# Performance work log

Measured on AMD Instinct MI355X. Metric: run time of the kernel, lower is better.

## Reference

```python
import jax, jax.numpy as jnp
import numpy as np

SEQ, BS, DIM = 2048, 2, 256
G, NQ = 2, 8           # n_keys groups, n_queries total
SUB = NQ // G          # queries per group
EPS = 1e-5


def _ln(x, gamma, beta):
    m = jnp.mean(x, axis=-1, keepdims=True)
    v = jnp.mean(jnp.square(x - m), axis=-1, keepdims=True)
    return (x - m) * jax.lax.rsqrt(v + EPS) * gamma + beta


def setup_inputs() -> dict:
    key = jax.random.key(0)
    ks = jax.random.split(key, 16)
    s = 0.02
    return {
        "x":   jax.random.normal(ks[0], (SEQ, BS, DIM), jnp.float32),
        # block layernorms
        "g0": jnp.ones((DIM,), jnp.float32), "b0": jnp.zeros((DIM,), jnp.float32),
        "g1": jnp.ones((DIM,), jnp.float32), "b1": jnp.zeros((DIM,), jnp.float32),
        # attention q/k layernorm (norm_kvs=True)
        "gn": jnp.ones((DIM,), jnp.float32), "bn": jnp.zeros((DIM,), jnp.float32),
        # attention projections (torch Linear: weight [out,in])
        "wk": jax.random.normal(ks[1], (DIM * G, DIM), jnp.float32) * s,
        "bk": jnp.zeros((DIM * G,), jnp.float32),
        "wv": jax.random.normal(ks[2], (DIM * G, DIM), jnp.float32) * s,
        "bv": jnp.zeros((DIM * G,), jnp.float32),
        "wq": jax.random.normal(ks[3], (DIM * NQ, DIM), jnp.float32) * s,
        "bq": jnp.zeros((DIM * NQ,), jnp.float32),
        "wo": jax.random.normal(ks[4], (DIM, DIM * NQ), jnp.float32) * s,
        "bo": jnp.zeros((DIM,), jnp.float32),
        # FFN: BayesLora(dim,2dim) -> relu -> BayesLora(2dim,dim), eval == plain linear
        "w1": jax.random.normal(ks[5], (2 * DIM, DIM), jnp.float32) * s,
        "bf1": jnp.zeros((2 * DIM,), jnp.float32),
        "w2": jax.random.normal(ks[6], (DIM, 2 * DIM), jnp.float32) * s,
        "bf2": jnp.zeros((DIM,), jnp.float32),
    }


def reference(x, g0, b0, g1, b1, gn, bn, wk, bk, wv, bv, wq, bq, wo, bo, w1, bf1, w2, bf2):
    seq, bs, dim = x.shape
    # --- attention (pre-norm) ---
    h = _ln(x, g0, b0)                                        # s b d
    K = (h @ wk.T + bk).reshape(seq, bs, G, dim)              # s b g i
    V = (h @ wv.T + bv).reshape(seq, bs, G, dim)              # s b g i
    Q = (h @ wq.T + bq).reshape(seq, bs, G, SUB, dim)         # s b g u i
    K = _ln(K, gn, bn)
    Q = _ln(Q, gn, bn)
    scores = jnp.einsum('sbgui,tbgi->bgust', Q, K) / jnp.sqrt(jnp.float32(dim))
    neg = jnp.finfo(scores.dtype).min
    causal = jnp.tril(jnp.ones((seq, seq), bool))             # s1 >= s2 allowed
    scores = jnp.where(causal, scores, neg)
    probs = jax.nn.softmax(scores, axis=-1)                   # b g u s t
    out = jnp.einsum('bgust,tbgi->sbgui', probs, V)
    out = out.reshape(seq, bs, G * SUB * dim)                 # s b (g u i)
    x = x + (out @ wo.T + bo)
    # --- FFN (pre-norm) ---
    h2 = _ln(x, g1, b1)
    f = jax.nn.relu(h2 @ w1.T + bf1) @ w2.T + bf2
    return x + f
```

## Files before the change

kernel.cpp:

```cpp
#include <hip/hip_runtime.h>
#include <hip/hip_bf16.h>

#define SEQ  2048
#define BSZ  2
#define DIM  256
#define NG   2
#define NQH  8
#define SUBQ 4
#define ROWS (SEQ*BSZ)
#define NQKV 3072
#define QROW 6144

typedef unsigned int uint32;
typedef unsigned short ushort;
typedef __attribute__((ext_vector_type(8))) short short8;
typedef __attribute__((ext_vector_type(4))) float f32x4;

__device__ __forceinline__ float bflo(uint32 u){
  union { uint32 i; float f; } c; c.i = u << 16; return c.f;
}
__device__ __forceinline__ float bfhi(uint32 u){
  union { uint32 i; float f; } c; c.i = u & 0xffff0000u; return c.f;
}
__device__ __forceinline__ uint32 pack2(float a, float b){
  __hip_bfloat16 ha = __float2bfloat16(a);
  __hip_bfloat16 hb = __float2bfloat16(b);
  unsigned short ua, ub;
  __builtin_memcpy(&ua, &ha, 2);
  __builtin_memcpy(&ub, &hb, 2);
  return (uint32)ua | ((uint32)ub << 16);
}
__device__ __forceinline__ ushort bf16bits(float v){
  __hip_bfloat16 h = __float2bfloat16(v);
  ushort u; __builtin_memcpy(&u, &h, 2); return u;
}

__device__ __forceinline__ void dma16(const void* g, void* l) {
  __builtin_amdgcn_global_load_lds(
      (const __attribute__((address_space(1))) uint32*)g,
      (__attribute__((address_space(3))) uint32*)l, 16, 0, 0);
}

__global__ __launch_bounds__(256) void misc0(
    const float* __restrict__ wk, const float* __restrict__ wv,
    const float* __restrict__ wq, const float* __restrict__ wo,
    const float* __restrict__ w1, const float* __restrict__ w2,
    const float* __restrict__ bk, const float* __restrict__ bv,
    const float* __restrict__ bq,
    __hip_bfloat16* __restrict__ out, float* __restrict__ bc,
    const float* __restrict__ x, const float* __restrict__ g0,
    const float* __restrict__ b0, __hip_bfloat16* __restrict__ Hf)
{
  if (blockIdx.x < 771) {
    int u = blockIdx.x * 256 + threadIdx.x;
    if (u < 196608) {
      int lane = u & 63, col = lane & 15, quad = lane >> 4;
      const float* srcrow;
      if (u < 98304) {
        int n16 = u >> 9, kc = (u >> 6) & 7;
        int n = n16 * 16 + col;
        const float* m = (n < 512) ? (wk + (size_t)n * 256)
                       : (n < 1024) ? (wv + (size_t)(n - 512) * 256)
                                    : (wq + (size_t)(n - 1024) * 256);
        srcrow = m + kc * 32 + quad * 8;
      } else if (u < 163840) {
        int local = u - 98304;
        int n16 = local >> 12, kc = (local >> 6) & 63;
        srcrow = wo + (size_t)(n16 * 16 + col) * 2048 + kc * 32 + quad * 8;
      } else if (u < 180224) {
        int local = u - 163840;
        int n16 = local >> 9, kc = (local >> 6) & 7;
        srcrow = w1 + (size_t)(n16 * 16 + col) * 256 + kc * 32 + quad * 8;
      } else {
        int local = u - 180224;
        int n16 = local >> 10, kc = (local >> 6) & 15;
        srcrow = w2 + (size_t)(n16 * 16 + col) * 512 + kc * 32 + quad * 8;
      }
      float4 a = *(const float4*)srcrow;
      float4 b = *(const float4*)(srcrow + 4);
      uint4 st;
      st.x = pack2(a.x, a.y); st.y = pack2(a.z, a.w);
      st.z = pack2(b.x, b.y); st.w = pack2(b.z, b.w);
      *(uint4*)((ushort*)out + (size_t)u * 8) = st;
    } else {
      int bu = u - 196608;
      const float* src; int loc;
      if      (bu < 128) { src = bk; loc = bu; }
      else if (bu < 256) { src = bv; loc = bu - 128; }
      else               { src = bq; loc = bu - 256; }
      *(float4*)(bc + 4 * (size_t)bu) = *(const float4*)(src + 4 * (size_t)loc);
    }
  } else {
    int wave = threadIdx.x >> 6, lane = threadIdx.x & 63;
    int row = (blockIdx.x - 771) * 4 + wave;
    size_t base = (size_t)row * DIM + lane * 4;
    float4 v = *(const float4*)(x + base);
    float s  = v.x + v.y + v.z + v.w;
    float s2 = v.x*v.x + v.y*v.y + v.z*v.z + v.w*v.w;
    #pragma unroll
    for (int o = 1; o < 64; o <<= 1) {
      s  += __shfl_xor(s, o);
      s2 += __shfl_xor(s2, o);
    }
    float m = s * (1.0f / DIM);
    float rb = rsqrtf(s2 * (1.0f / DIM) - m * m + 1e-5f);
    float4 gm = *(const float4*)(g0 + lane * 4);
    float4 bt = *(const float4*)(b0 + lane * 4);
    uint2 st;
    st.x = pack2((v.x - m) * rb * gm.x + bt.x, (v.y - m) * rb * gm.y + bt.y);
    st.y = pack2((v.z - m) * rb * gm.z + bt.z, (v.w - m) * rb * gm.w + bt.w);
    int kc = lane >> 3, quad = (lane >> 1) & 3, jj = 4 * (lane & 1);
    int cid = (row >> 4) * 8 + kc;
    *(uint2*)((ushort*)Hf + (size_t)cid * 512 + (quad * 16 + (row & 15)) * 8 + jj) = st;
  }
}

__global__ __launch_bounds__(256) void ln_swz(
    __hip_bfloat16* __restrict__ QKV,
    const float* __restrict__ gamma, const float* __restrict__ beta,
    __hip_bfloat16* __restrict__ Kf, __hip_bfloat16* __restrict__ Vf)
{
  int j = blockIdx.x;
  if (j < 10240) {
    int wave = threadIdx.x >> 6, lane = threadIdx.x & 63;
    int idx = j * 4 + wave;
    size_t base;
    if (idx < 8192) base = (size_t)(idx >> 1) * NQKV + (idx & 1) * DIM;
    else {
      int qi = idx - 8192;
      base = (size_t)(qi >> 3) * NQKV + 2 * NG * DIM + (qi & 7) * DIM;
    }
    __hip_bfloat16* p = QKV + base + lane * 4;
    uint2 u = *(const uint2*)p;
    float v0 = bflo(u.x), v1 = bfhi(u.x), v2 = bflo(u.y), v3 = bfhi(u.y);
    float s  = v0 + v1 + v2 + v3;
    float s2 = v0*v0 + v1*v1 + v2*v2 + v3*v3;
    #pragma unroll
    for (int o = 1; o < 64; o <<= 1) {
      s  += __shfl_xor(s, o);
      s2 += __shfl_xor(s2, o);
    }
    float m = s * (1.0f / DIM);
    float rb = rsqrtf(s2 * (1.0f / DIM) - m * m + 1e-5f);
    float4 gm = *(const float4*)(gamma + lane * 4);
    float4 bt = *(const float4*)(beta + lane * 4);
    uint2 st;
    st.x = pack2((v0 - m) * rb * gm.x + bt.x, (v1 - m) * rb * gm.y + bt.y);
    st.y = pack2((v2 - m) * rb * gm.z + bt.z, (v3 - m) * rb * gm.w + bt.w);
    if (idx < 8192) {
      int r = idx >> 1, gg = idx & 1;
      int t = r >> 1, b = r & 1;
      int bg = b * NG + gg;
      int kt = t >> 5, tr = t & 31, tc = tr >> 4, col = tr & 15;
      int ks = lane >> 3, quad = (lane >> 1) & 3, jj = 4 * (lane & 1);
      int cid = (bg * 64 + kt) * 16 + tc * 8 + ks;
      *(uint2*)((ushort*)Kf + (size_t)cid * 512 + (quad * 16 + col) * 8 + jj) = st;
    } else {
      *(uint2*)p = st;
    }
  } else {
    __shared__ ushort T[64][72];
    int vb = j - 10240;
    int t0 = (vb & 31) * 64, d0 = ((vb >> 5) & 3) * 64, bg = vb >> 7;
    int b = bg >> 1, g = bg & 1;
    int tid = threadIdx.x;
    int tr = tid >> 2, c4 = (tid & 3) * 16;
    const ushort* src = (const ushort*)QKV + ((size_t)(t0 + tr) * BSZ + b) * NQKV
                      + NG * DIM + g * DIM + d0 + c4;
    uint4 a0 = *(const uint4*)src;
    uint4 a1 = *(const uint4*)(src + 8);
    *(uint4*)&T[tr][c4]     = a0;
    *(uint4*)&T[tr][c4 + 8] = a1;
    __syncthreads();
    #pragma unroll
    for (int k2 = 0; k2 < 2; ++k2) {
      int u = tid * 2 + k2;
      int tt = u >> 8, di = (u >> 6) & 3, qd = (u >> 4) & 3, cl = u & 15;
      ushort tmp[8];
      #pragma unroll
      for (int e = 0; e < 8; ++e) tmp[e] = T[tt * 32 + qd * 8 + e][di * 16 + cl];
      int kt = (t0 >> 5) + tt;
      int dc = (d0 >> 4) + di;
      *(uint4*)((ushort*)Vf + (((size_t)(bg * 64 + kt) * 16 + dc) << 9) + (qd * 16 + cl) * 8)
          = *(uint4*)tmp;
    }
  }
}

template<int GN, int RELU, int OUTMODE, int AFRAG>
__global__ __launch_bounds__(256) void gemm_mfma(
    const __hip_bfloat16* __restrict__ A,
    const __hip_bfloat16* __restrict__ W,
    const float* __restrict__ bias,
    const float* __restrict__ resid,
    void* __restrict__ outp,
    int M, int N, int K)
{
  constexpr int WCH = GN / 16;
  constexpr int MC  = (GN == 128) ? 4 : 2;
  __shared__ __align__(16) ushort AS[2][4096];
  __shared__ __align__(16) ushort WS[2][WCH * 512];

  const int tid = threadIdx.x;
  const int wave = tid >> 6, lane = tid & 63;
  const int col = lane & 15, quad = lane >> 4;
  const int wm = (GN == 128) ? (wave >> 1) : wave;
  const int wn = (GN == 128) ? (wave & 1) : 0;
  const int bn0 = blockIdx.x * GN;
  const int bm0 = blockIdx.y * 128;
  const bool SPLIT = (OUTMODE == 2 || OUTMODE == 4);
  const int Keff  = SPLIT ? (K / gridDim.z) : K;
  const int kbase = SPLIT ? blockIdx.z * Keff : 0;
  const int kiters = Keff >> 5;

  f32x4 acc[MC][4];
  #pragma unroll
  for (int mc = 0; mc < MC; ++mc)
    #pragma unroll
    for (int nc = 0; nc < 4; ++nc)
      acc[mc][nc] = (f32x4){0.f, 0.f, 0.f, 0.f};

  auto stage = [&](int it, int bufi) {
    int k0 = kbase + it * 32;
    #pragma unroll
    for (int c = 0; c < 2; ++c) {
      int ch = wave * 2 + c;
      if (AFRAG)
        dma16((const ushort*)A + ((((size_t)(bm0 >> 4) + ch) * (K >> 5) + (k0 >> 5)) << 9) + lane * 8,
              &AS[bufi][ch * 512]);
      else
        dma16((const ushort*)A + (size_t)(bm0 + ch * 16 + col) * K + k0 + quad * 8,
              &AS[bufi][ch * 512]);
    }
    #pragma unroll
    for (int c = 0; c < WCH / 4; ++c) {
      int ch = wave * (WCH / 4) + c;
      dma16((const ushort*)W + (((size_t)((bn0 >> 4) + ch) * (K >> 5) + (k0 >> 5)) << 9) + lane * 8,
            &WS[bufi][ch * 512]);
    }
  };

  stage(0, 0);
  for (int it = 0; it < kiters; ++it) {
    int cur = it & 1;
    __syncthreads();
    if (it + 1 < kiters) stage(it + 1, 1 - cur);
    short8 af[MC], bf_[4];
    #pragma unroll
    for (int mc = 0; mc < MC; ++mc)
      af[mc] = *(const short8*)&AS[cur][(wm * MC + mc) * 512 + lane * 8];
    #pragma unroll
    for (int nc = 0; nc < 4; ++nc)
      bf_[nc] = *(const short8*)&WS[cur][(wn * 4 + nc) * 512 + lane * 8];
    #pragma unroll
    for (int mc = 0; mc < MC; ++mc)
      #pragma unroll
      for (int nc = 0; nc < 4; ++nc)
        acc[mc][nc] = __builtin_amdgcn_mfma_f32_16x16x32_bf16(af[mc], bf_[nc], acc[mc][nc], 0, 0, 0);
  }

  #pragma unroll
  for (int nc = 0; nc < 4; ++nc) {
    int n = bn0 + wn * 64 + nc * 16 + col;
    float bv = 0.f;
    if (OUTMODE == 0 || OUTMODE == 1 || OUTMODE == 3) bv = bias[n];
    #pragma unroll
    for (int mc = 0; mc < MC; ++mc) {
      #pragma unroll
      for (int reg = 0; reg < 4; ++reg) {
        int m = bm0 + wm * (MC * 16) + mc * 16 + quad * 4 + reg;
        float v = acc[mc][nc][reg] + bv;
        if ((OUTMODE == 0 || OUTMODE == 1 || OUTMODE == 3) && resid)
          v += resid[(size_t)m * N + n];
        if (RELU) v = fmaxf(v, 0.f);
        if (OUTMODE == 0)
          ((__hip_bfloat16*)outp)[(size_t)m * N + n] = __float2bfloat16(v);
        else if (OUTMODE == 1)
          ((float*)outp)[(size_t)m * N + n] = v;
        else if (OUTMODE == 2)
          ((float*)outp)[(size_t)blockIdx.z * M * N + (size_t)m * N + n] = v;
        else if (OUTMODE == 3) {
          int cid = (m >> 4) * (N >> 5) + (n >> 5);
          int kl = n & 31;
          ((ushort*)outp)[(size_t)cid * 512 + ((kl >> 3) * 16 + (m & 15)) * 8 + (kl & 7)] = bf16bits(v);
        } else {
          ((ushort*)outp)[(size_t)blockIdx.z * M * N + (size_t)m * N + n] = bf16bits(v);
        }
      }
    }
  }
}

__global__ __launch_bounds__(256) void combine2(
    const ushort* __restrict__ P, const float* __restrict__ bias,
    const float* __restrict__ resid, float* __restrict__ out, int MN)
{
  int i4 = (blockIdx.x * 256 + threadIdx.x) * 4;
  uint2 a = *(const uint2*)(P + i4);
  uint2 b = *(const uint2*)(P + MN + i4);
  float4 r = *(const float4*)(resid + i4);
  float4 bb = *(const float4*)(bias + (i4 & (DIM - 1)));
  float4 o;
  o.x = bflo(a.x) + bflo(b.x) + r.x + bb.x;
  o.y = bfhi(a.x) + bfhi(b.x) + r.y + bb.y;
  o.z = bflo(a.y) + bflo(b.y) + r.z + bb.z;
  o.w = bfhi(a.y) + bfhi(b.y) + r.w + bb.w;
  *(float4*)(out + i4) = o;
}

__global__ __launch_bounds__(256) void combine_ln4(
    const ushort* __restrict__ P, const float* __restrict__ bias,
    const float* __restrict__ resid, float* __restrict__ X2,
    const float* __restrict__ gamma, const float* __restrict__ beta,
    __hip_bfloat16* __restrict__ H2f)
{
  const int MN = ROWS * DIM;
  int wave = threadIdx.x >> 6, lane = threadIdx.x & 63;
  int row = blockIdx.x * 4 + wave;
  size_t i = (size_t)row * DIM + lane * 4;
  uint2 a = *(const uint2*)(P + i);
  uint2 b = *(const uint2*)(P + MN + i);
  uint2 c = *(const uint2*)(P + 2 * (size_t)MN + i);
  uint2 d = *(const uint2*)(P + 3 * (size_t)MN + i);
  float4 r = *(const float4*)(resid + i);
  float4 bb = *(const float4*)(bias + lane * 4);
  float4 v;
  v.x = bflo(a.x) + bflo(b.x) + bflo(c.x) + bflo(d.x) + r.x + bb.x;
  v.y = bfhi(a.x) + bfhi(b.x) + bfhi(c.x) + bfhi(d.x) + r.y + bb.y;
  v.z = bflo(a.y) + bflo(b.y) + bflo(c.y) + bflo(d.y) + r.z + bb.z;
  v.w = bfhi(a.y) + bfhi(b.y) + bfhi(c.y) + bfhi(d.y) + r.w + bb.w;
  *(float4*)(X2 + i) = v;
  float s  = v.x + v.y + v.z + v.w;
  float s2 = v.x*v.x + v.y*v.y + v.z*v.z + v.w*v.w;
  #pragma unroll
  for (int o = 1; o < 64; o <<= 1) {
    s  += __shfl_xor(s, o);
    s2 += __shfl_xor(s2, o);
  }
  float m = s * (1.0f / DIM);
  float rb = rsqrtf(s2 * (1.0f / DIM) - m * m + 1e-5f);
  float4 gm = *(const float4*)(gamma + lane * 4);
  float4 bt = *(const float4*)(beta + lane * 4);
  uint2 st;
  st.x = pack2((v.x - m) * rb * gm.x + bt.x, (v.y - m) * rb * gm.y + bt.y);
  st.y = pack2((v.z - m) * rb * gm.z + bt.z, (v.w - m) * rb * gm.w + bt.w);
  int kc = lane >> 3, quad = (lane >> 1) & 3, jj = 4 * (lane & 1);
  int cid = (row >> 4) * 8 + kc;
  *(uint2*)((ushort*)H2f + (size_t)cid * 512 + (quad * 16 + (row & 15)) * 8 + jj) = st;
}

__global__ __launch_bounds__(256, 2) void attn_mfma(
    const __hip_bfloat16* __restrict__ QKV,
    const __hip_bfloat16* __restrict__ Kf,
    const __hip_bfloat16* __restrict__ Vf,
    __hip_bfloat16* __restrict__ Obf,
    __hip_bfloat16* __restrict__ Op1f,
    float* __restrict__ Lp)
{
  __shared__ __align__(16) ushort KS[2][8192];
  __shared__ __align__(16) ushort VS[2][8192];
  __shared__ __align__(16) ushort Pw[4][1280];

  const int tid  = threadIdx.x;
  const int wave = tid >> 6, lane = tid & 63;
  const int col  = lane & 15, quad = lane >> 4;
  const int head = blockIdx.x & 15;
  const int w    = blockIdx.x >> 4;
  int qb, z, split, nit, k0;
  if (w < 24) { qb = 15 - (w >> 1); z = w & 1; split = 1; nit = 2 * qb + 2; k0 = z * nit; }
  else        { qb = 27 - w;        z = 0;     split = 0; nit = 4 * qb + 4; k0 = 0; }

  const int b = head >> 3, hq = head & 7, g = hq >> 2;
  const int bg = b * NG + g;
  const int qw0 = qb * 128 + wave * 32;

  short8 qf[2][8];
  #pragma unroll
  for (int mc = 0; mc < 2; ++mc) {
    int s = qw0 + mc * 16 + col;
    const ushort* qp = (const ushort*)QKV + (size_t)s * QROW + b * NQKV
                     + 2 * NG * DIM + hq * DIM + quad * 8;
    #pragma unroll
    for (int ks = 0; ks < 8; ++ks)
      qf[mc][ks] = *(const short8*)(qp + ks * 32);
  }

  short8 onesf;
  #pragma unroll
  for (int i = 0; i < 8; ++i) onesf[i] = (short)0x3F80;

  f32x4 o[2][16];
  #pragma unroll
  for (int mc = 0; mc < 2; ++mc)
    #pragma unroll
    for (int dc = 0; dc < 16; ++dc)
      o[mc][dc] = (f32x4){0.f, 0.f, 0.f, 0.f};
  float l_s[2][4] = {{0.f}};

  auto stage = [&](int i, int bufi) {
    int kt = k0 + i;
    const ushort* kb = (const ushort*)Kf + (((size_t)bg * 64 + kt) << 13);
    const ushort* vb = (const ushort*)Vf + (((size_t)bg * 64 + kt) << 13);
    #pragma unroll
    for (int cc = 0; cc < 4; ++cc) {
      int nk = wave * 4 + cc;
      dma16(kb + (nk << 9) + lane * 8, &KS[bufi][nk * 512]);
      dma16(vb + (nk << 9) + lane * 8, &VS[bufi][nk * 512]);
    }
  };

  stage(0, 0);
  for (int i = 0; i < nit; ++i) {
    int cur = i & 1;
    __syncthreads();
    if (i + 1 < nit) stage(i + 1, 1 - cur);
    int kt = k0 + i;
    if (kt * 32 > qw0 + 31) continue;

    f32x4 sf[2][2];
    #pragma unroll
    for (int mc = 0; mc < 2; ++mc)
      #pragma unroll
      for (int tc = 0; tc < 2; ++tc)
        sf[mc][tc] = (f32x4){0.f, 0.f, 0.f, 0.f};
    #pragma unroll
    for (int ks = 0; ks < 8; ++ks) {
      short8 kb0 = *(const short8*)&KS[cur][ks * 512 + lane * 8];
      short8 kb1 = *(const short8*)&KS[cur][(8 + ks) * 512 + lane * 8];
      sf[0][0] = __builtin_amdgcn_mfma_f32_16x16x32_bf16(qf[0][ks], kb0, sf[0][0], 0, 0, 0);
      sf[0][1] = __builtin_amdgcn_mfma_f32_16x16x32_bf16(qf[0][ks], kb1, sf[0][1], 0, 0, 0);
      sf[1][0] = __builtin_amdgcn_mfma_f32_16x16x32_bf16(qf[1][ks], kb0, sf[1][0], 0, 0, 0);
      sf[1][1] = __builtin_amdgcn_mfma_f32_16x16x32_bf16(qf[1][ks], kb1, sf[1][1], 0, 0, 0);
    }

    const bool dm = (kt * 32 + 31) > qw0;
    #pragma unroll
    for (int mc = 0; mc < 2; ++mc)
      #pragma unroll
      for (int tc = 0; tc < 2; ++tc)
        #pragma unroll
        for (int reg = 0; reg < 4; ++reg) {
          float p = __expf(sf[mc][tc][reg] * 0.0625f);
          if (dm) {
            int tg = kt * 32 + tc * 16 + col;
            int sg = qw0 + mc * 16 + quad * 4 + reg;
            if (tg > sg) p = 0.f;
          }
          Pw[wave][(mc * 16 + quad * 4 + reg) * 40 + tc * 16 + col] = bf16bits(p);
        }

    short8 pa0 = *(const short8*)&Pw[wave][col * 40 + quad * 8];
    short8 pa1 = *(const short8*)&Pw[wave][(16 + col) * 40 + quad * 8];

    f32x4 zz = (f32x4){0.f, 0.f, 0.f, 0.f};
    f32x4 ps0 = __builtin_amdgcn_mfma_f32_16x16x32_bf16(pa0, onesf, zz, 0, 0, 0);
    f32x4 ps1 = __builtin_amdgcn_mfma_f32_16x16x32_bf16(pa1, onesf, zz, 0, 0, 0);
    #pragma unroll
    for (int r = 0; r < 4; ++r) { l_s[0][r] += ps0[r]; l_s[1][r] += ps1[r]; }

    #pragma unroll
    for (int dc = 0; dc < 16; ++dc) {
      short8 vb = *(const short8*)&VS[cur][dc * 512 + lane * 8];
      o[0][dc] = __builtin_amdgcn_mfma_f32_16x16x32_bf16(pa0, vb, o[0][dc], 0, 0, 0);
      o[1][dc] = __builtin_amdgcn_mfma_f32_16x16x32_bf16(pa1, vb, o[1][dc], 0, 0, 0);
    }
  }

  const int colh = col >> 3, coll = col & 7;
  #pragma unroll
  for (int mc = 0; mc < 2; ++mc)
    #pragma unroll
    for (int reg = 0; reg < 4; ++reg) {
      int s = qw0 + mc * 16 + quad * 4 + reg;
      int m = s * BSZ + b;
      int m16 = m >> 4, ml = m & 15;
      float inv = 1.0f / l_s[mc][reg];
      if (!split) {
        #pragma unroll
        for (int dc = 0; dc < 16; ++dc) {
          int cid = m16 * 64 + hq * 8 + (dc >> 1);
          int qt = (dc & 1) * 2 + colh;
          Obf[(size_t)cid * 512 + (qt * 16 + ml) * 8 + coll] =
              __float2bfloat16(o[mc][dc][reg] * inv);
        }
      } else {
        #pragma unroll
        for (int dc = 0; dc < 16; ++dc) {
          int qt = (dc & 1) * 2 + colh;
          size_t off;
          __hip_bfloat16* dst;
          if (z == 0) {
            dst = Obf;  off = ((size_t)(m16 * 64 + hq * 8 + (dc >> 1))) * 512;
          } else {
            dst = Op1f; off = ((size_t)((m16 - 64) * 64 + hq * 8 + (dc >> 1))) * 512;
          }
          dst[off + (qt * 16 + ml) * 8 + coll] = __float2bfloat16(o[mc][dc][reg]);
        }
        if (col == 0) Lp[(z * 1536 + (s - 512)) * 16 + head] = l_s[mc][reg];
      }
    }
}

__global__ __launch_bounds__(256) void attn_norm(
    __hip_bfloat16* __restrict__ Obf, const __hip_bfloat16* __restrict__ Op1f,
    const float* __restrict__ Lp)
{
  int i8 = blockIdx.x * 256 + threadIdx.x;
  int cidr = i8 >> 6;
  int lane = i8 & 63;
  int m16r = cidr >> 6, kc = cidr & 63;
  int m = (m16r + 64) * 16 + (lane & 15);
  int k = kc * 32 + (lane >> 4) * 8;
  int s = m >> 1, b = m & 1, hq = k >> 8;
  int row = s - 512, head = b * 8 + hq;
  float inv = 1.0f / (Lp[row * 16 + head] + Lp[(1536 + row) * 16 + head]);
  ushort* a = (ushort*)Obf + (((size_t)(m16r + 64) * 64 + kc) << 9) + lane * 8;
  const ushort* c = (const ushort*)Op1f + (((size_t)m16r * 64 + kc) << 9) + lane * 8;
  uint4 ua = *(const uint4*)a;
  uint4 uc = *(const uint4*)c;
  uint4 st;
  st.x = pack2((bflo(ua.x) + bflo(uc.x)) * inv, (bfhi(ua.x) + bfhi(uc.x)) * inv);
  st.y = pack2((bflo(ua.y) + bflo(uc.y)) * inv, (bfhi(ua.y) + bfhi(uc.y)) * inv);
  st.z = pack2((bflo(ua.z) + bflo(uc.z)) * inv, (bfhi(ua.z) + bfhi(uc.z)) * inv);
  st.w = pack2((bflo(ua.w) + bflo(uc.w)) * inv, (bfhi(ua.w) + bfhi(uc.w)) * inv);
  *(uint4*)a = st;
}

extern "C" void kernel_launch(void* const* d_in, const int* in_sizes, int n_in,
                              void* d_out, int out_size, void* d_ws, size_t ws_size,
                              hipStream_t stream)
{
  const float* x   = (const float*)d_in[0];
  const float* g0  = (const float*)d_in[1];
  const float* b0  = (const float*)d_in[2];
  const float* g1  = (const float*)d_in[3];
  const float* b1  = (const float*)d_in[4];
  const float* gn  = (const float*)d_in[5];
  const float* bn  = (const float*)d_in[6];
  const float* wk  = (const float*)d_in[7];
  const float* bk  = (const float*)d_in[8];
  const float* wv  = (const float*)d_in[9];
  const float* bv  = (const float*)d_in[10];
  const float* wq  = (const float*)d_in[11];
  const float* bq  = (const float*)d_in[12];
  const float* wo  = (const float*)d_in[13];
  const float* bo  = (const float*)d_in[14];
  const float* w1  = (const float*)d_in[15];
  const float* bf1 = (const float*)d_in[16];
  const float* w2  = (const float*)d_in[17];
  const float* bf2 = (const float*)d_in[18];

  char* ws = (char*)d_ws;
  const size_t MB = 1024 * 1024;
  __hip_bfloat16* QKV = (__hip_bfloat16*)(ws);
  __hip_bfloat16* Pwo = (__hip_bfloat16*)(ws);
  __hip_bfloat16* Pw2 = (__hip_bfloat16*)(ws + 8  * MB);
  float*          X2  = (float*)         (ws + 16 * MB);
  __hip_bfloat16* H2f = (__hip_bfloat16*)(ws + 20 * MB);
  __hip_bfloat16* F1f = (__hip_bfloat16*)(ws + 22 * MB);
  __hip_bfloat16* Hf  = (__hip_bfloat16*)(ws + 24 * MB);
  __hip_bfloat16* Kf  = (__hip_bfloat16*)(ws + 24 * MB);
  __hip_bfloat16* Vf  = (__hip_bfloat16*)(ws + 28 * MB);
  __hip_bfloat16* Obf = (__hip_bfloat16*)(ws + 32 * MB);
  __hip_bfloat16* Op1f= (__hip_bfloat16*)(ws + 48 * MB);
  float*          BC  = (float*)         (ws + 60 * MB + 768 * 1024);
  float*          Lp  = (float*)         (ws + 60 * MB + 800 * 1024);
  __hip_bfloat16* WB  = (__hip_bfloat16*)(ws + 61 * MB);

  __hip_bfloat16* woB = WB + 786432;
  __hip_bfloat16* w1B = WB + 1310720;
  __hip_bfloat16* w2B = WB + 1441792;

  misc0<<<1795, 256, 0, stream>>>(wk, wv, wq, wo, w1, w2, bk, bv, bq, WB, BC, x, g0, b0, Hf);
  gemm_mfma<128,0,0,1><<<dim3(NQKV/128, ROWS/128), 256, 0, stream>>>(Hf, WB, BC, nullptr, QKV, ROWS, NQKV, DIM);
  ln_swz<<<12288, 256, 0, stream>>>(QKV, gn, bn, Kf, Vf);
  attn_mfma<<<448, 256, 0, stream>>>(QKV, Kf, Vf, Obf, Op1f, Lp);
  attn_norm<<<3072, 256, 0, stream>>>(Obf, Op1f, Lp);
  gemm_mfma<64,0,4,1><<<dim3(DIM/64, ROWS/128, 4), 256, 0, stream>>>(Obf, woB, nullptr, nullptr, Pwo, ROWS, DIM, NQH*DIM);
  combine_ln4<<<ROWS / 4, 256, 0, stream>>>((const ushort*)Pwo, bo, x, X2, g1, b1, H2f);
  gemm_mfma<64,1,3,1><<<dim3((2*DIM)/64, ROWS/128), 256, 0, stream>>>(H2f, w1B, bf1, nullptr, F1f, ROWS, 2*DIM, DIM);
  gemm_mfma<64,0,4,1><<<dim3(DIM/64, ROWS/128, 2), 256, 0, stream>>>(F1f, w2B, nullptr, nullptr, Pw2, ROWS, DIM, 2*DIM);
  combine2<<<ROWS*DIM/1024, 256, 0, stream>>>((const ushort*)Pw2, bf2, X2, (float*)d_out, ROWS*DIM);
}
```

Baseline: 249.0 us.

## Rebalance causal attention work with table-driven 3-way KV splits

Replaces the fixed 2-way split schedule of the attention kernel with a constant lookup table that assigns query blocks, KV split index, start offset and iteration count. The longest query blocks are split three ways, giving 512 blocks of roughly equal length, ordered longest-first and interleaved across heads. The third partial output goes into unused parts of the QKV buffer, and the normalise kernel sums up to three partials. The aim is less tail imbalance across the grid. The cost is a third partial buffer, extra reads in the merge, and reliance on QKV regions not being read concurrently (the restrict qualifier was dropped from QKV).

```diff
diff --git a/kernel.cpp b/kernel.cpp
--- a/kernel.cpp
+++ b/kernel.cpp
@@ -349,12 +349,19 @@
   *(uint2*)((ushort*)H2f + (size_t)cid * 512 + (quad * 16 + (row & 15)) * 8 + jj) = st;
 }
 
+__constant__ int C_NIT[32] = {22,22,22,21,21,20,20,20,20,20,20,19,19,18,18,18,18,17,17,16,16,16,16,16,16,14,14,12,12,12, 8, 4};
+__constant__ int C_QB [32] = {10,10,15,15,15, 4, 9, 9,14,14,14,13,13,13, 8, 8,12,12,12, 3, 7, 7,11,11,11, 6, 6, 2, 5, 5, 1, 0};
+__constant__ int C_Z  [32] = { 0, 1, 0, 1, 2, 0, 0, 1, 0, 1, 2, 0, 1, 2, 0, 1, 0, 1, 2, 0, 0, 1, 0, 1, 2, 0, 1, 0, 0, 1, 0, 0};
+__constant__ int C_K0 [32] = { 0,22, 0,22,43, 0, 0,20, 0,20,40, 0,19,38, 0,18, 0,18,35, 0, 0,16, 0,16,32, 0,14, 0, 0,12, 0, 0};
+__constant__ int C_SP [32] = { 1, 1, 1, 1, 1, 0, 1, 1, 1, 1, 1, 1, 1, 1, 1, 1, 1, 1, 1, 0, 1, 1, 1, 1, 1, 1, 1, 0, 1, 1, 0, 0};
+
 __global__ __launch_bounds__(256, 2) void attn_mfma(
-    const __hip_bfloat16* __restrict__ QKV,
+    const __hip_bfloat16* QKV,
     const __hip_bfloat16* __restrict__ Kf,
     const __hip_bfloat16* __restrict__ Vf,
     __hip_bfloat16* __restrict__ Obf,
     __hip_bfloat16* __restrict__ Op1f,
+    ushort* Op2q,
     float* __restrict__ Lp)
 {
   __shared__ __align__(16) ushort KS[2][8192];
@@ -364,11 +371,17 @@
   const int tid  = threadIdx.x;
   const int wave = tid >> 6, lane = tid & 63;
   const int col  = lane & 15, quad = lane >> 4;
-  const int head = blockIdx.x & 15;
-  const int w    = blockIdx.x >> 4;
-  int qb, z, split, nit, k0;
-  if (w < 24) { qb = 15 - (w >> 1); z = w & 1; split = 1; nit = 2 * qb + 2; k0 = z * nit; }
-  else        { qb = 27 - w;        z = 0;     split = 0; nit = 4 * qb + 4; k0 = 0; }
+
+  const int bid = blockIdx.x;
+  const int x8 = bid & 7, j = bid >> 3;
+  const int hpar = j & 1;
+  const int rank = (j < 32) ? (j >> 1) : (31 - ((j - 32) >> 1));
+  const int head = x8 * 2 + hpar;
+  const int qb  = C_QB[rank];
+  const int z   = C_Z[rank];
+  const int nit = C_NIT[rank];
+  const int k0  = C_K0[rank];
+  const int split = C_SP[rank];
 
   const int b = head >> 3, hq = head & 7, g = hq >> 2;
   const int bg = b * NG + g;
@@ -474,8 +487,8 @@
       int s = qw0 + mc * 16 + quad * 4 + reg;
       int m = s * BSZ + b;
       int m16 = m >> 4, ml = m & 15;
-      float inv = 1.0f / l_s[mc][reg];
       if (!split) {
+        float inv = 1.0f / l_s[mc][reg];
         #pragma unroll
         for (int dc = 0; dc < 16; ++dc) {
           int cid = m16 * 64 + hq * 8 + (dc >> 1);
@@ -487,42 +500,59 @@
         #pragma unroll
         for (int dc = 0; dc < 16; ++dc) {
           int qt = (dc & 1) * 2 + colh;
-          size_t off;
-          __hip_bfloat16* dst;
+          int el = (qt * 16 + ml) * 8 + coll;
+          float v = o[mc][dc][reg];
           if (z == 0) {
-            dst = Obf;  off = ((size_t)(m16 * 64 + hq * 8 + (dc >> 1))) * 512;
+            Obf[((size_t)(m16 * 64 + hq * 8 + (dc >> 1))) * 512 + el] = __float2bfloat16(v);
+          } else if (z == 1) {
+            Op1f[((size_t)((m16 - 80) * 64 + hq * 8 + (dc >> 1))) * 512 + el] = __float2bfloat16(v);
           } else {
-            dst = Op1f; off = ((size_t)((m16 - 64) * 64 + hq * 8 + (dc >> 1))) * 512;
+            size_t o2 = ((size_t)((m16 - 176) * 64 + hq * 8 + (dc >> 1))) * 512 + el;
+            Op2q[(o2 >> 10) * 6144 + (o2 & 1023)] = bf16bits(v);
           }
-          dst[off + (qt * 16 + ml) * 8 + coll] = __float2bfloat16(o[mc][dc][reg]);
         }
-        if (col == 0) Lp[(z * 1536 + (s - 512)) * 16 + head] = l_s[mc][reg];
+        if (col == 0) Lp[((size_t)z * 2048 + s) * 16 + head] = l_s[mc][reg];
       }
     }
 }
 
 __global__ __launch_bounds__(256) void attn_norm(
     __hip_bfloat16* __restrict__ Obf, const __hip_bfloat16* __restrict__ Op1f,
-    const float* __restrict__ Lp)
+    const ushort* __restrict__ Op2q, const float* __restrict__ Lp)
 {
   int i8 = blockIdx.x * 256 + threadIdx.x;
   int cidr = i8 >> 6;
   int lane = i8 & 63;
   int m16r = cidr >> 6, kc = cidr & 63;
-  int m = (m16r + 64) * 16 + (lane & 15);
+  int m16 = m16r + 80;
+  int m = m16 * 16 + (lane & 15);
   int k = kc * 32 + (lane >> 4) * 8;
   int s = m >> 1, b = m & 1, hq = k >> 8;
-  int row = s - 512, head = b * 8 + hq;
-  float inv = 1.0f / (Lp[row * 16 + head] + Lp[(1536 + row) * 16 + head]);
-  ushort* a = (ushort*)Obf + (((size_t)(m16r + 64) * 64 + kc) << 9) + lane * 8;
+  int head = b * 8 + hq;
+  float l = Lp[(size_t)s * 16 + head] + Lp[(size_t)(2048 + s) * 16 + head];
+  ushort* a = (ushort*)Obf + (((size_t)m16 * 64 + kc) << 9) + lane * 8;
   const ushort* c = (const ushort*)Op1f + (((size_t)m16r * 64 + kc) << 9) + lane * 8;
   uint4 ua = *(const uint4*)a;
   uint4 uc = *(const uint4*)c;
+  float v0 = bflo(ua.x) + bflo(uc.x), v1 = bfhi(ua.x) + bfhi(uc.x);
+  float v2 = bflo(ua.y) + bflo(uc.y), v3 = bfhi(ua.y) + bfhi(uc.y);
+  float v4 = bflo(ua.z) + bflo(uc.z), v5 = bfhi(ua.z) + bfhi(uc.z);
+  float v6 = bflo(ua.w) + bflo(uc.w), v7 = bfhi(ua.w) + bfhi(uc.w);
+  if (s >= 1408) {
+    l += Lp[(size_t)(4096 + s) * 16 + head];
+    size_t o2 = (((size_t)(m16 - 176) * 64 + kc) << 9) + lane * 8;
+    uint4 ue = *(const uint4*)(Op2q + (o2 >> 10) * 6144 + (o2 & 1023));
+    v0 += bflo(ue.x); v1 += bfhi(ue.x);
+    v2 += bflo(ue.y); v3 += bfhi(ue.y);
+    v4 += bflo(ue.z); v5 += bfhi(ue.z);
+    v6 += bflo(ue.w); v7 += bfhi(ue.w);
+  }
+  float inv = 1.0f / l;
   uint4 st;
-  st.x = pack2((bflo(ua.x) + bflo(uc.x)) * inv, (bfhi(ua.x) + bfhi(uc.x)) * inv);
-  st.y = pack2((bflo(ua.y) + bflo(uc.y)) * inv, (bfhi(ua.y) + bfhi(uc.y)) * inv);
-  st.z = pack2((bflo(ua.z) + bflo(uc.z)) * inv, (bfhi(ua.z) + bfhi(uc.z)) * inv);
-  st.w = pack2((bflo(ua.w) + bflo(uc.w)) * inv, (bfhi(ua.w) + bfhi(uc.w)) * inv);
+  st.x = pack2(v0 * inv, v1 * inv);
+  st.y = pack2(v2 * inv, v3 * inv);
+  st.z = pack2(v4 * inv, v5 * inv);
+  st.w = pack2(v6 * inv, v7 * inv);
   *(uint4*)a = st;
 }
 
@@ -563,8 +593,8 @@
   __hip_bfloat16* Vf  = (__hip_bfloat16*)(ws + 28 * MB);
   __hip_bfloat16* Obf = (__hip_bfloat16*)(ws + 32 * MB);
   __hip_bfloat16* Op1f= (__hip_bfloat16*)(ws + 48 * MB);
-  float*          BC  = (float*)         (ws + 60 * MB + 768 * 1024);
-  float*          Lp  = (float*)         (ws + 60 * MB + 800 * 1024);
+  float*          BC  = (float*)         (ws + 59 * MB);
+  float*          Lp  = (float*)         (ws + 59 * MB + 64 * 1024);
   __hip_bfloat16* WB  = (__hip_bfloat16*)(ws + 61 * MB);
 
   __hip_bfloat16* woB = WB + 786432;
@@ -574,8 +604,8 @@
   misc0<<<1795, 256, 0, stream>>>(wk, wv, wq, wo, w1, w2, bk, bv, bq, WB, BC, x, g0, b0, Hf);
   gemm_mfma<128,0,0,1><<<dim3(NQKV/128, ROWS/128), 256, 0, stream>>>(Hf, WB, BC, nullptr, QKV, ROWS, NQKV, DIM);
   ln_swz<<<12288, 256, 0, stream>>>(QKV, gn, bn, Kf, Vf);
-  attn_mfma<<<448, 256, 0, stream>>>(QKV, Kf, Vf, Obf, Op1f, Lp);
-  attn_norm<<<3072, 256, 0, stream>>>(Obf, Op1f, Lp);
+  attn_mfma<<<512, 256, 0, stream>>>(QKV, Kf, Vf, Obf, Op1f, (ushort*)QKV, Lp);
+  attn_norm<<<2816, 256, 0, stream>>>(Obf, Op1f, (const ushort*)QKV, Lp);
   gemm_mfma<64,0,4,1><<<dim3(DIM/64, ROWS/128, 4), 256, 0, stream>>>(Obf, woB, nullptr, nullptr, Pwo, ROWS, DIM, NQH*DIM);
   combine_ln4<<<ROWS / 4, 256, 0, stream>>>((const ushort*)Pwo, bo, x, X2, g1, b1, H2f);
   gemm_mfma<64,1,3,1><<<dim3((2*DIM)/64, ROWS/128), 256, 0, stream>>>(H2f, w1B, bf1, nullptr, F1f, ROWS, 2*DIM, DIM);
```

After: 243.7 us. -2.2%, faster.
